# Optimization experiments

Hardware: AMD Instinct MI355X
Metric: run time of the kernel (lower is better)

The kernel has to match this reference:

```python
import jax, jax.numpy as jnp
import numpy as np

N_NODES = 50000
M_ITEMS = 5000
D_FEAT = 64      # graph node feature dim (input_size)
D_HID = 32       # input_size // 2
D_EMB = 64       # embedding_size = output_size
N_EDGES = 1200000
BATCH = 4096


def _sage_conv(h, src, dst, W_l, b_l, W_r, n_nodes):
    # PyG SAGEConv (mean aggr, root_weight=True):
    # out_i = W_l @ mean_{j in N(i)} h_j + b_l + W_r @ h_i
    msg = h[src]                                              # [E, Din]
    agg = jax.ops.segment_sum(msg, dst, num_segments=n_nodes)  # [N, Din]
    deg = jax.ops.segment_sum(jnp.ones((src.shape[0],), h.dtype), dst,
                              num_segments=n_nodes)
    agg = agg / jnp.maximum(deg, 1.0)[:, None]
    return agg @ W_l.T + b_l + h @ W_r.T


def setup_inputs() -> dict:
    key = jax.random.key(0)
    ks = jax.random.split(key, 12)
    x = jax.random.randint(ks[0], (BATCH,), 0, N_NODES)
    node_x = jax.random.normal(ks[1], (N_NODES, D_FEAT), dtype=jnp.float32)
    edge_index = jax.random.randint(ks[2], (2, N_EDGES), 0, N_NODES)
    rating_mat = jax.random.uniform(ks[3], (N_NODES, M_ITEMS), dtype=jnp.float32)
    s = 0.05
    W_enc = jax.random.normal(ks[4], (D_EMB, M_ITEMS), dtype=jnp.float32) * s
    b_enc = jnp.zeros((D_EMB,), jnp.float32)
    W_dec = jax.random.normal(ks[5], (M_ITEMS, D_EMB), dtype=jnp.float32) * s
    b_dec = jnp.zeros((M_ITEMS,), jnp.float32)
    Wl1 = jax.random.normal(ks[6], (D_HID, D_FEAT), dtype=jnp.float32) * s
    bl1 = jnp.zeros((D_HID,), jnp.float32)
    Wr1 = jax.random.normal(ks[7], (D_HID, D_FEAT), dtype=jnp.float32) * s
    Wl2 = jax.random.normal(ks[8], (D_EMB, D_HID), dtype=jnp.float32) * s
    bl2 = jnp.zeros((D_EMB,), jnp.float32)
    Wr2 = jax.random.normal(ks[9], (D_EMB, D_HID), dtype=jnp.float32) * s
    return {"x": x, "node_x": node_x, "edge_index": edge_index,
            "rating_mat": rating_mat, "W_enc": W_enc, "b_enc": b_enc,
            "W_dec": W_dec, "b_dec": b_dec, "Wl1": Wl1, "bl1": bl1,
            "Wr1": Wr1, "Wl2": Wl2, "bl2": bl2, "Wr2": Wr2}


def reference(x, node_x, edge_index, rating_mat, W_enc, b_enc, W_dec, b_dec,
              Wl1, bl1, Wr1, Wl2, bl2, Wr2):
    src, dst = edge_index[0], edge_index[1]
    # Graph branch (training path, dropout omitted for determinism)
    h = _sage_conv(node_x, src, dst, Wl1, bl1, Wr1, N_NODES)   # [N, D_HID]
    h = jax.nn.relu(h)
    emb_all = _sage_conv(h, src, dst, Wl2, bl2, Wr2, N_NODES)  # [N, D_EMB]
    emb_graph = emb_all[x]                                      # [B, D_EMB]
    # Autoencoder branch
    items = rating_mat[x]                                       # [B, M]
    emb_ae = items @ W_enc.T + b_enc                            # [B, D_EMB]
    out = jax.nn.sigmoid(emb_graph + emb_ae)                    # method='add'
    out = jax.nn.sigmoid(out @ W_dec.T + b_dec)                 # [B, M]
    return out
```

## Files before the change

kernel.cpp:

```cpp
#include <hip/hip_runtime.h>
#include <math.h>

#define N_NODES 50000
#define M_ITEMS 5000
#define D_FEAT 64
#define D_HID 32
#define D_EMB 64
#define N_EDGES 1200000
#define BATCH 4096
#define CAP 80
#define KCH 10
#define KW  500
#define MCH 313

typedef unsigned short u16;
typedef unsigned int u32;
typedef __attribute__((ext_vector_type(8))) short bf16x8;
typedef __attribute__((ext_vector_type(4))) float f32x4;

__device__ __forceinline__ float sigmoidf_(float z) {
    return 1.0f / (1.0f + __expf(-z));
}
__device__ __forceinline__ u16 f2bf(float f) {
    u32 b = __float_as_uint(f);
    b += 0x7FFFu + ((b >> 16) & 1u);
    return (u16)(b >> 16);
}

#define FILL_BLOCKS  ((N_EDGES + 255) / 256)
#define XW_BLOCKS    ((N_NODES * D_HID + 255) / 256)
#define TR_BLOCKS    ((D_EMB * M_ITEMS + 255) / 256)
#define WB_THREADS   (MCH * 2 * 64)
#define WB_BLOCKS    ((WB_THREADS + 255) / 256)

__global__ __launch_bounds__(256)
void k_mega1(const int* __restrict__ src, const int* __restrict__ dst,
             int* __restrict__ cursor, int* __restrict__ slot,
             const float* __restrict__ Wenc, float* __restrict__ WencT,
             const float* __restrict__ node_x, const float* __restrict__ Wl1,
             float* __restrict__ y1, const float* __restrict__ Wdec,
             uint4* __restrict__ WdecB) {
    __shared__ float wsT[D_FEAT * D_HID];
    const int bid = blockIdx.x;
    if (bid < FILL_BLOCKS) {
        int e = bid * 256 + threadIdx.x;
        if (e < N_EDGES) {
            int dn = dst[e];
            int pos = atomicAdd(&cursor[dn], 1);
            if (pos < CAP) slot[(size_t)dn * CAP + pos] = src[e];
        }
        return;
    }
    if (bid < FILL_BLOCKS + XW_BLOCKS) {
        for (int j = threadIdx.x; j < D_FEAT * D_HID; j += 256) {
            int c = j / D_FEAT, k = j % D_FEAT;
            wsT[k * D_HID + c] = Wl1[j];
        }
        __syncthreads();
        int idx = (bid - FILL_BLOCKS) * 256 + threadIdx.x;
        if (idx >= N_NODES * D_HID) return;
        int r = idx >> 5, c = idx & 31;
        const float* xp = node_x + (size_t)r * D_FEAT;
        float s = 0.f;
#pragma unroll
        for (int k = 0; k < D_FEAT; k += 4) {
            float4 xv = *reinterpret_cast<const float4*>(xp + k);
            s = fmaf(xv.x, wsT[(k + 0) * D_HID + c], s);
            s = fmaf(xv.y, wsT[(k + 1) * D_HID + c], s);
            s = fmaf(xv.z, wsT[(k + 2) * D_HID + c], s);
            s = fmaf(xv.w, wsT[(k + 3) * D_HID + c], s);
        }
        y1[idx] = s;
        return;
    }
    if (bid < FILL_BLOCKS + XW_BLOCKS + TR_BLOCKS) {
        int idx = (bid - FILL_BLOCKS - XW_BLOCKS) * 256 + threadIdx.x;
        if (idx >= D_EMB * M_ITEMS) return;
        int e = idx & 63, m = idx >> 6;
        WencT[idx] = Wenc[(size_t)e * M_ITEMS + m];
        return;
    }
    {
        int g = (bid - FILL_BLOCKS - XW_BLOCKS - TR_BLOCKS) * 256 + threadIdx.x;
        if (g >= WB_THREADS) return;
        int lane = g & 63, sq = g >> 6;
        int step = sq & 1, chunk = sq >> 1;
        int m = chunk * 16 + (lane & 15);
        int k0 = step * 32 + ((lane >> 4) << 3);
        u32 p0 = 0, p1 = 0, p2 = 0, p3 = 0;
        if (m < M_ITEMS) {
            const float* wp = Wdec + (size_t)m * 64 + k0;
            float4 f0 = *reinterpret_cast<const float4*>(wp);
            float4 f1 = *reinterpret_cast<const float4*>(wp + 4);
            p0 = (u32)f2bf(f0.x) | ((u32)f2bf(f0.y) << 16);
            p1 = (u32)f2bf(f0.z) | ((u32)f2bf(f0.w) << 16);
            p2 = (u32)f2bf(f1.x) | ((u32)f2bf(f1.y) << 16);
            p3 = (u32)f2bf(f1.z) | ((u32)f2bf(f1.w) << 16);
        }
        WdecB[g] = make_uint4(p0, p1, p2, p3);
    }
}

__global__ __launch_bounds__(256)
void k_node1(const float* __restrict__ node_x, const float* __restrict__ y1,
             const int* __restrict__ cursor, const int* __restrict__ slot,
             const float* __restrict__ Wr1, const float* __restrict__ bl1,
             float* __restrict__ h) {
    __shared__ float wt[D_FEAT * D_HID];
    __shared__ float xsh[8][64];
    const int tid = threadIdx.x;
    for (int j = tid; j < D_HID * D_FEAT; j += 256) {
        int c = j >> 6, k = j & 63;
        wt[k * D_HID + c] = Wr1[j];
    }
    const int nb = blockIdx.x * 8;
    for (int j = tid; j < 8 * 64; j += 256)
        xsh[j >> 6][j & 63] = node_x[(size_t)(nb + (j >> 6)) * D_FEAT + (j & 63)];
    __syncthreads();
    const int lane = tid & 63, wv = tid >> 6;
    const int k32 = lane & 31, hi = lane >> 5;
    const int nA = nb + wv * 2, nB = nA + 1;
    const int dgfA = cursor[nA], dgfB = cursor[nB];
    const int dgA = min(dgfA, CAP), dgB = min(dgfB, CAP);
    const int mx = max(dgA, dgB);
    const int* slA = slot + (size_t)nA * CAP;
    const int* slB = slot + (size_t)nB * CAP;
    const int dgv = hi ? dgB : dgA;
    float a0 = 0.f, a1 = 0.f, a2 = 0.f, a3 = 0.f;
    for (int j = 0; j < mx; j += 4) {
#pragma unroll
        for (int i = 0; i < 4; ++i) {
            int sA = (j + i < dgA) ? slA[j + i] : 0;
            int sB = (j + i < dgB) ? slB[j + i] : 0;
            int nbr = hi ? sB : sA;
            float v = y1[(size_t)nbr * D_HID + k32];
            float vm = (j + i < dgv) ? v : 0.f;
            if (i == 0) a0 += vm; else if (i == 1) a1 += vm;
            else if (i == 2) a2 += vm; else a3 += vm;
        }
    }
    float g = (a0 + a1) + (a2 + a3);
    const int my = wv * 2 + hi;
    const float dgfv = (float)(hi ? dgfB : dgfA);
    float s = g / fmaxf(dgfv, 1.f) + bl1[k32];
#pragma unroll
    for (int k = 0; k < D_FEAT; k += 4) {
        float4 xv = *reinterpret_cast<const float4*>(&xsh[my][k]);
        s = fmaf(xv.x, wt[(k + 0) * D_HID + k32], s);
        s = fmaf(xv.y, wt[(k + 1) * D_HID + k32], s);
        s = fmaf(xv.z, wt[(k + 2) * D_HID + k32], s);
        s = fmaf(xv.w, wt[(k + 3) * D_HID + k32], s);
    }
    h[(size_t)(nb + my) * D_HID + k32] = fmaxf(s, 0.f);
}

__global__ __launch_bounds__(512)
void k_enc_part(const int* __restrict__ x, const float* __restrict__ rating,
                const float* __restrict__ WencT, float* __restrict__ part) {
    __shared__ float sm[8192];
    __shared__ int ns[16];
    const int tid = threadIdx.x, lane = tid & 63, wv = tid >> 6;
    const int rb = blockIdx.x * 16;
    const int ky = blockIdx.y;
    if (tid < 16) ns[tid] = x[rb + tid];
    __syncthreads();
    int nh[16];
#pragma unroll
    for (int i = 0; i < 16; ++i)
        nh[i] = __builtin_amdgcn_readfirstlane(ns[i]);
    for (int j4 = tid; j4 < 2000; j4 += 512) {
        int row = j4 / 125, c4 = j4 - row * 125;
        float4 v = *reinterpret_cast<const float4*>(
            rating + (size_t)nh[row] * M_ITEMS + ky * KW + c4 * 4);
        *reinterpret_cast<float4*>(&sm[row * KW + c4 * 4]) = v;
    }
    __syncthreads();
    float acc[16];
#pragma unroll
    for (int i = 0; i < 16; ++i) acc[i] = 0.f;
    for (int g = wv; g < 125; g += 8) {
        int ml = g * 4, gm = ky * KW + ml;
        float w0 = WencT[(size_t)(gm + 0) * 64 + lane];
        float w1 = WencT[(size_t)(gm + 1) * 64 + lane];
        float w2 = WencT[(size_t)(gm + 2) * 64 + lane];
        float w3 = WencT[(size_t)(gm + 3) * 64 + lane];
#pragma unroll
        for (int r = 0; r < 16; ++r) {
            float4 rv = *reinterpret_cast<const float4*>(&sm[r * KW + ml]);
            acc[r] = fmaf(rv.x, w0, acc[r]);
            acc[r] = fmaf(rv.y, w1, acc[r]);
            acc[r] = fmaf(rv.z, w2, acc[r]);
            acc[r] = fmaf(rv.w, w3, acc[r]);
        }
    }
    __syncthreads();
#pragma unroll
    for (int r = 0; r < 16; ++r) sm[(wv * 16 + r) * 64 + lane] = acc[r];
    __syncthreads();
#pragma unroll
    for (int half = 0; half < 2; ++half) {
        int r = wv * 2 + half;
        float s = 0.f;
#pragma unroll
        for (int w = 0; w < 8; ++w) s += sm[(w * 16 + r) * 64 + lane];
        part[((size_t)ky * BATCH + rb + r) * 64 + lane] = s;
    }
}

__global__ __launch_bounds__(512)
void k_comb(const int* __restrict__ x, const float* __restrict__ part,
            const float* __restrict__ benc, const int* __restrict__ cursor,
            const int* __restrict__ slot, const float* __restrict__ h,
            const float* __restrict__ Wl2, const float* __restrict__ bl2,
            const float* __restrict__ Wr2, u16* __restrict__ emb_bf) {
    __shared__ float wl2t[D_HID * D_EMB];
    __shared__ float wr2t[D_HID * D_EMB];
    __shared__ float aggl[8][D_HID];
    __shared__ float hl[8][D_HID];
    __shared__ int ns[8];
    const int tid = threadIdx.x, lane = tid & 63, wv = tid >> 6;
    const int rb = blockIdx.x * 8;
    if (tid < 8) ns[tid] = x[rb + tid];
    for (int j = tid; j < D_EMB * D_HID; j += 512) {
        int e = j >> 5, k = j & 31;
        wl2t[k * D_EMB + e] = Wl2[j];
        wr2t[k * D_EMB + e] = Wr2[j];
    }
    __syncthreads();
    const int row = rb + wv;
    const int node = __builtin_amdgcn_readfirstlane(ns[wv]);
    float ae = benc[lane];
#pragma unroll
    for (int ky = 0; ky < KCH; ++ky)
        ae += part[((size_t)ky * BATCH + row) * 64 + lane];
    const int k32 = lane & 31, hi = lane >> 5;
    const int dgf = cursor[node];
    const int dg = min(dgf, CAP);
    const int* sl = slot + (size_t)node * CAP;
    float a0 = 0.f, a1 = 0.f, a2 = 0.f, a3 = 0.f;
    for (int t = 0; t < dg; t += 8) {
#pragma unroll
        for (int i = 0; i < 4; ++i) {
            int j2 = t + 2 * i;
            int sE = (j2 < dg) ? sl[j2] : 0;
            int sO = (j2 + 1 < dg) ? sl[j2 + 1] : 0;
            int nbr = hi ? sO : sE;
            float v = h[(size_t)nbr * D_HID + k32];
            float vm = (j2 + hi < dg) ? v : 0.f;
            if (i == 0) a0 += vm; else if (i == 1) a1 += vm;
            else if (i == 2) a2 += vm; else a3 += vm;
        }
    }
    float g = (a0 + a1) + (a2 + a3);
    g += __shfl(g, lane ^ 32, 64);
    if (lane < 32) {
        aggl[wv][k32] = g / fmaxf((float)dgf, 1.f);
        hl[wv][k32] = h[(size_t)node * D_HID + k32];
    }
    float ge = bl2[lane];
#pragma unroll
    for (int k = 0; k < D_HID; ++k)
        ge = fmaf(aggl[wv][k], wl2t[k * D_EMB + lane], ge);
#pragma unroll
    for (int k = 0; k < D_HID; ++k)
        ge = fmaf(hl[wv][k], wr2t[k * D_EMB + lane], ge);
    emb_bf[(size_t)row * D_EMB + lane] = f2bf(sigmoidf_(ge + ae));
}

__global__ __launch_bounds__(256)
void k_dec(const u16* __restrict__ emb_bf, const bf16x8* __restrict__ WdecB,
           const float* __restrict__ bdec, float* __restrict__ out) {
    const int tid = threadIdx.x, lane = tid & 63, wv = tid >> 6;
    const int q = blockIdx.x * 4 + wv;
    if (q >= MCH) return;
    const int r0 = blockIdx.y * 16;
    const int row = r0 + (lane & 15);
    const int kq = (lane >> 4) << 3;
    const u16* ea = emb_bf + (size_t)row * 64 + kq;
    bf16x8 A0 = *reinterpret_cast<const bf16x8*>(ea);
    bf16x8 A1 = *reinterpret_cast<const bf16x8*>(ea + 32);
    bf16x8 B0 = WdecB[(size_t)(q * 2 + 0) * 64 + lane];
    bf16x8 B1 = WdecB[(size_t)(q * 2 + 1) * 64 + lane];
    f32x4 c = {0.f, 0.f, 0.f, 0.f};
    c = __builtin_amdgcn_mfma_f32_16x16x32_bf16(A0, B0, c, 0, 0, 0);
    c = __builtin_amdgcn_mfma_f32_16x16x32_bf16(A1, B1, c, 0, 0, 0);
    const int m = q * 16 + (lane & 15);
    if (m < M_ITEMS) {
        float bb = bdec[m];
        const int rbase = r0 + (lane >> 4) * 4;
#pragma unroll
        for (int i = 0; i < 4; ++i)
            out[(size_t)(rbase + i) * M_ITEMS + m] = sigmoidf_(c[i] + bb);
    }
}

extern "C" void kernel_launch(void* const* d_in, const int* in_sizes, int n_in,
                              void* d_out, int out_size, void* d_ws, size_t ws_size,
                              hipStream_t stream) {
    const int*   x      = (const int*)d_in[0];
    const float* node_x = (const float*)d_in[1];
    const int*   ei     = (const int*)d_in[2];
    const float* rating = (const float*)d_in[3];
    const float* Wenc   = (const float*)d_in[4];
    const float* benc   = (const float*)d_in[5];
    const float* Wdec   = (const float*)d_in[6];
    const float* bdec   = (const float*)d_in[7];
    const float* Wl1    = (const float*)d_in[8];
    const float* bl1    = (const float*)d_in[9];
    const float* Wr1    = (const float*)d_in[10];
    const float* Wl2    = (const float*)d_in[11];
    const float* bl2    = (const float*)d_in[12];
    const float* Wr2    = (const float*)d_in[13];
    const int* src = ei;
    const int* dst = ei + N_EDGES;

    char* w = (char*)d_ws;
    int*   cursor = (int*)w;   w += (size_t)N_NODES * 4;
    int*   slot   = (int*)w;   w += (size_t)N_NODES * CAP * 4;
    float* y1     = (float*)w; w += (size_t)N_NODES * D_HID * 4;
    float* h      = (float*)w; w += (size_t)N_NODES * D_HID * 4;
    u16*   emb_bf = (u16*)w;   w += (size_t)BATCH * D_EMB * 2;
    float* WencT  = (float*)w; w += (size_t)M_ITEMS * D_EMB * 4;
    float* part   = (float*)w; w += (size_t)KCH * BATCH * D_EMB * 4;
    uint4* WdecB  = (uint4*)w; w += (size_t)WB_THREADS * 16;

    hipMemsetAsync(cursor, 0, (size_t)N_NODES * 4, stream);

    k_mega1<<<FILL_BLOCKS + XW_BLOCKS + TR_BLOCKS + WB_BLOCKS, 256, 0, stream>>>(
        src, dst, cursor, slot, Wenc, WencT, node_x, Wl1, y1, Wdec, WdecB);
    k_node1<<<N_NODES / 8, 256, 0, stream>>>(
        node_x, y1, cursor, slot, Wr1, bl1, h);
    dim3 genc(BATCH / 16, KCH);
    k_enc_part<<<genc, 512, 0, stream>>>(x, rating, WencT, part);
    k_comb<<<BATCH / 8, 512, 0, stream>>>(
        x, part, benc, cursor, slot, h, Wl2, bl2, Wr2, emb_bf);
    dim3 gdec((MCH + 3) / 4, BATCH / 16);
    k_dec<<<gdec, 256, 0, stream>>>(emb_bf, (const bf16x8*)WdecB, bdec,
                                    (float*)d_out);
}
```

Measured before the change: 296.6 us.

## Store neighbor slots as 16-bit indices and tile decoder over four row blocks

The adjacency slot table now holds 16-bit node indices instead of 32-bit ones. This halves its footprint and the bytes moved by the edge fill and by the neighbor gathers in both SAGE layers, and is only valid because the node count fits in 16 bits. The decoder kernel now loops each wave over four 16-row tiles while keeping the same weight fragments and bias in registers. This cuts the grid to a quarter of its previous size and removes repeated B-fragment loads, in exchange for more serial work per wave.

```diff
diff --git a/kernel.cpp b/kernel.cpp
--- a/kernel.cpp
+++ b/kernel.cpp
@@ -35,7 +35,7 @@
 
 __global__ __launch_bounds__(256)
 void k_mega1(const int* __restrict__ src, const int* __restrict__ dst,
-             int* __restrict__ cursor, int* __restrict__ slot,
+             int* __restrict__ cursor, u16* __restrict__ slot,
              const float* __restrict__ Wenc, float* __restrict__ WencT,
              const float* __restrict__ node_x, const float* __restrict__ Wl1,
              float* __restrict__ y1, const float* __restrict__ Wdec,
@@ -47,7 +47,7 @@
         if (e < N_EDGES) {
             int dn = dst[e];
             int pos = atomicAdd(&cursor[dn], 1);
-            if (pos < CAP) slot[(size_t)dn * CAP + pos] = src[e];
+            if (pos < CAP) slot[(size_t)dn * CAP + pos] = (u16)src[e];
         }
         return;
     }
@@ -103,7 +103,7 @@
 
 __global__ __launch_bounds__(256)
 void k_node1(const float* __restrict__ node_x, const float* __restrict__ y1,
-             const int* __restrict__ cursor, const int* __restrict__ slot,
+             const int* __restrict__ cursor, const u16* __restrict__ slot,
              const float* __restrict__ Wr1, const float* __restrict__ bl1,
              float* __restrict__ h) {
     __shared__ float wt[D_FEAT * D_HID];
@@ -123,15 +123,15 @@
     const int dgfA = cursor[nA], dgfB = cursor[nB];
     const int dgA = min(dgfA, CAP), dgB = min(dgfB, CAP);
     const int mx = max(dgA, dgB);
-    const int* slA = slot + (size_t)nA * CAP;
-    const int* slB = slot + (size_t)nB * CAP;
+    const u16* slA = slot + (size_t)nA * CAP;
+    const u16* slB = slot + (size_t)nB * CAP;
     const int dgv = hi ? dgB : dgA;
     float a0 = 0.f, a1 = 0.f, a2 = 0.f, a3 = 0.f;
     for (int j = 0; j < mx; j += 4) {
 #pragma unroll
         for (int i = 0; i < 4; ++i) {
-            int sA = (j + i < dgA) ? slA[j + i] : 0;
-            int sB = (j + i < dgB) ? slB[j + i] : 0;
+            int sA = (j + i < dgA) ? (int)slA[j + i] : 0;
+            int sB = (j + i < dgB) ? (int)slB[j + i] : 0;
             int nbr = hi ? sB : sA;
             float v = y1[(size_t)nbr * D_HID + k32];
             float vm = (j + i < dgv) ? v : 0.f;
@@ -210,7 +210,7 @@
 __global__ __launch_bounds__(512)
 void k_comb(const int* __restrict__ x, const float* __restrict__ part,
             const float* __restrict__ benc, const int* __restrict__ cursor,
-            const int* __restrict__ slot, const float* __restrict__ h,
+            const u16* __restrict__ slot, const float* __restrict__ h,
             const float* __restrict__ Wl2, const float* __restrict__ bl2,
             const float* __restrict__ Wr2, u16* __restrict__ emb_bf) {
     __shared__ float wl2t[D_HID * D_EMB];
@@ -236,14 +236,14 @@
     const int k32 = lane & 31, hi = lane >> 5;
     const int dgf = cursor[node];
     const int dg = min(dgf, CAP);
-    const int* sl = slot + (size_t)node * CAP;
+    const u16* sl = slot + (size_t)node * CAP;
     float a0 = 0.f, a1 = 0.f, a2 = 0.f, a3 = 0.f;
     for (int t = 0; t < dg; t += 8) {
 #pragma unroll
         for (int i = 0; i < 4; ++i) {
             int j2 = t + 2 * i;
-            int sE = (j2 < dg) ? sl[j2] : 0;
-            int sO = (j2 + 1 < dg) ? sl[j2 + 1] : 0;
+            int sE = (j2 < dg) ? (int)sl[j2] : 0;
+            int sO = (j2 + 1 < dg) ? (int)sl[j2 + 1] : 0;
             int nbr = hi ? sO : sE;
             float v = h[(size_t)nbr * D_HID + k32];
             float vm = (j2 + hi < dg) ? v : 0.f;
@@ -273,24 +273,27 @@
     const int tid = threadIdx.x, lane = tid & 63, wv = tid >> 6;
     const int q = blockIdx.x * 4 + wv;
     if (q >= MCH) return;
-    const int r0 = blockIdx.y * 16;
-    const int row = r0 + (lane & 15);
-    const int kq = (lane >> 4) << 3;
-    const u16* ea = emb_bf + (size_t)row * 64 + kq;
-    bf16x8 A0 = *reinterpret_cast<const bf16x8*>(ea);
-    bf16x8 A1 = *reinterpret_cast<const bf16x8*>(ea + 32);
     bf16x8 B0 = WdecB[(size_t)(q * 2 + 0) * 64 + lane];
     bf16x8 B1 = WdecB[(size_t)(q * 2 + 1) * 64 + lane];
-    f32x4 c = {0.f, 0.f, 0.f, 0.f};
-    c = __builtin_amdgcn_mfma_f32_16x16x32_bf16(A0, B0, c, 0, 0, 0);
-    c = __builtin_amdgcn_mfma_f32_16x16x32_bf16(A1, B1, c, 0, 0, 0);
     const int m = q * 16 + (lane & 15);
-    if (m < M_ITEMS) {
-        float bb = bdec[m];
-        const int rbase = r0 + (lane >> 4) * 4;
-#pragma unroll
-        for (int i = 0; i < 4; ++i)
-            out[(size_t)(rbase + i) * M_ITEMS + m] = sigmoidf_(c[i] + bb);
+    const bool mok = (m < M_ITEMS);
+    const float bb = mok ? bdec[m] : 0.f;
+    const int kq = (lane >> 4) << 3;
+#pragma unroll
+    for (int rt = 0; rt < 4; ++rt) {
+        const int r0 = blockIdx.y * 64 + rt * 16;
+        const u16* ea = emb_bf + (size_t)(r0 + (lane & 15)) * 64 + kq;
+        bf16x8 A0 = *reinterpret_cast<const bf16x8*>(ea);
+        bf16x8 A1 = *reinterpret_cast<const bf16x8*>(ea + 32);
+        f32x4 c = {0.f, 0.f, 0.f, 0.f};
+        c = __builtin_amdgcn_mfma_f32_16x16x32_bf16(A0, B0, c, 0, 0, 0);
+        c = __builtin_amdgcn_mfma_f32_16x16x32_bf16(A1, B1, c, 0, 0, 0);
+        if (mok) {
+            const int rbase = r0 + (lane >> 4) * 4;
+#pragma unroll
+            for (int i = 0; i < 4; ++i)
+                out[(size_t)(rbase + i) * M_ITEMS + m] = sigmoidf_(c[i] + bb);
+        }
     }
 }
 
@@ -316,7 +319,7 @@
 
     char* w = (char*)d_ws;
     int*   cursor = (int*)w;   w += (size_t)N_NODES * 4;
-    int*   slot   = (int*)w;   w += (size_t)N_NODES * CAP * 4;
+    u16*   slot   = (u16*)w;   w += (size_t)N_NODES * CAP * 2;
     float* y1     = (float*)w; w += (size_t)N_NODES * D_HID * 4;
     float* h      = (float*)w; w += (size_t)N_NODES * D_HID * 4;
     u16*   emb_bf = (u16*)w;   w += (size_t)BATCH * D_EMB * 2;
@@ -334,7 +337,7 @@
     k_enc_part<<<genc, 512, 0, stream>>>(x, rating, WencT, part);
     k_comb<<<BATCH / 8, 512, 0, stream>>>(
         x, part, benc, cursor, slot, h, Wl2, bl2, Wr2, emb_bf);
-    dim3 gdec((MCH + 3) / 4, BATCH / 16);
+    dim3 gdec((MCH + 3) / 4, BATCH / 64);
     k_dec<<<gdec, 256, 0, stream>>>(emb_bf, (const bf16x8*)WdecB, bdec,
                                     (float*)d_out);
 }
```

New measurement: 317.6 us. 7.1% more time.
